# Optimization experiments

Hardware: AMD Instinct MI355X
Metric: run time of the kernel (lower is better)

## Reference

```python
import jax, jax.numpy as jnp
import numpy as np

NEG_INF = -jnp.inf


def _rope(x, cos, sin):
    # x: (B, S, H, D); cos/sin: (1, S, 1, D//2)
    xr = x.reshape(*x.shape[:-1], -1, 2)
    x1, x2 = xr[..., 0], xr[..., 1]  # (B, S, H, D//2) each
    # faithful to source: concat halves along last axis, same total size D
    return jnp.concatenate([x1 * cos - x2 * sin, x1 * sin + x2 * cos], axis=-1)


def setup_inputs() -> dict:
    B, S, D, H, Ld = 2, 2048, 2048, 16, 128
    key = jax.random.key(0)
    ks = jax.random.split(key, 6)
    sc = 1.0 / np.sqrt(D)
    return {
        "x": jax.random.normal(ks[0], (B, S, D), jnp.float32),
        "attn_mask": jnp.ones((B, S), jnp.int32),
        "Wq": jax.random.normal(ks[1], (D, H * Ld), jnp.float32) * sc,
        "bq": jnp.zeros((H * Ld,), jnp.float32),
        "Wk": jax.random.normal(ks[2], (D, H * Ld), jnp.float32) * sc,
        "bk": jnp.zeros((H * Ld,), jnp.float32),
        "Wv": jax.random.normal(ks[3], (D, H * Ld), jnp.float32) * sc,
        "bv": jnp.zeros((H * Ld,), jnp.float32),
        "Wo": jax.random.normal(ks[4], (H * Ld, D), jnp.float32) * sc,
        "bo": jnp.zeros((D,), jnp.float32),
        "num_heads": H,
    }


def reference(x, attn_mask, Wq, bq, Wk, bk, Wv, bv, Wo, bo, num_heads):
    B, S, D = x.shape
    H = int(num_heads)
    Ld = Wq.shape[1] // H
    base = 10000

    q = (x @ Wq + bq).reshape(B, S, H, Ld)
    k = (x @ Wk + bk).reshape(B, S, H, Ld)
    v = (x @ Wv + bv).reshape(B, S, H, Ld)

    # rotary tables (match RotaryEmbedding.setup, sliced to seq_len)
    inv_freq = 1.0 / base ** (2 * jnp.arange(0, Ld // 2) / Ld)
    angles = jnp.arange(S)[:, None] * inv_freq[None, :]  # (S, Ld//2)
    cos = jnp.cos(angles)[None, :, None, :].astype(x.dtype)
    sin = jnp.sin(angles)[None, :, None, :].astype(x.dtype)
    q = _rope(q, cos, sin)
    k = _rope(k, cos, sin)

    q = jnp.transpose(q, (0, 2, 1, 3))  # (B, H, S, Ld)
    k = jnp.transpose(k, (0, 2, 1, 3))
    v = jnp.transpose(v, (0, 2, 1, 3))

    scale = jnp.sqrt(jnp.float32(Ld)).astype(x.dtype)
    scores = jnp.einsum('bnqd,bnkd->bnqk', q, k) / scale  # (B, H, S, S)

    # faithful mask from source: keep where arange[None,:] >= arange[:,None]
    row_idx = jnp.arange(S)[None, :]
    col_idx = jnp.arange(S)[:, None]
    keep = row_idx >= col_idx  # (S, S)
    scores = jnp.where(keep[None, None, :, :], scores, NEG_INF)

    # padding mask applied over the QUERY axis, as in source: (B,1,S,1)
    scores = jnp.where(attn_mask[:, None, :, None] > 0, scores, NEG_INF)

    attn = jax.nn.softmax(scores, axis=-1)
    attended = jnp.einsum('bnqk,bnkd->bnqd', attn, v)
    attended = jnp.transpose(attended, (0, 2, 1, 3)).reshape(B, S, H * Ld)
    return attended @ Wo + bo
```

## Files before the change

kernel.cpp:

```cpp
#include <hip/hip_runtime.h>
#include <math.h>

typedef __bf16 bf16x8 __attribute__((ext_vector_type(8)));
typedef float f32x4 __attribute__((ext_vector_type(4)));

#define MFMA_BF16(a,b,c) __builtin_amdgcn_mfma_f32_16x16x32_bf16((a),(b),(c),0,0,0)

static constexpr int S_LEN = 2048;
static constexpr int DM    = 2048;
static constexpr int NHEAD = 16;
static constexpr int LDH   = 128;
static constexpr int BATCH = 2;

__device__ __forceinline__ unsigned short f2bf(float f) {
    unsigned u = __float_as_uint(f);
    u += 0x7fffu + ((u >> 16) & 1u);
    return (unsigned short)(u >> 16);
}
__device__ __forceinline__ float bf2f(unsigned short h) {
    return __uint_as_float(((unsigned)h) << 16);
}
__device__ __forceinline__ float fexp2(float x) {
#if __has_builtin(__builtin_amdgcn_exp2f)
    return __builtin_amdgcn_exp2f(x);
#else
    return exp2f(x);
#endif
}

__device__ __forceinline__ void ld_lds16(const void* g, void* l) {
    __builtin_amdgcn_global_load_lds(
        (const __attribute__((address_space(1))) unsigned int*)g,
        (__attribute__((address_space(3))) unsigned int*)l, 16, 0, 0);
}

__global__ void convert_f32_bf16(const float* __restrict__ in,
                                 unsigned short* __restrict__ out, int n4) {
    int idx = blockIdx.x * blockDim.x + threadIdx.x;
    if (idx >= n4) return;
    float4 v = reinterpret_cast<const float4*>(in)[idx];
    unsigned lo = (unsigned)f2bf(v.x) | ((unsigned)f2bf(v.y) << 16);
    unsigned hi = (unsigned)f2bf(v.z) | ((unsigned)f2bf(v.w) << 16);
    reinterpret_cast<uint2*>(out)[idx] = make_uint2(lo, hi);
}

__global__ void wconv_t4(const float* __restrict__ W0, const float* __restrict__ W1,
                         const float* __restrict__ W2, const float* __restrict__ W3,
                         unsigned short* __restrict__ O0, unsigned short* __restrict__ O1,
                         unsigned short* __restrict__ O2, unsigned short* __restrict__ O3) {
    __shared__ unsigned short tile[32][33];
    int z = blockIdx.z;
    const float* W = (z == 0) ? W0 : (z == 1) ? W1 : (z == 2) ? W2 : W3;
    unsigned short* Wt = (z == 0) ? O0 : (z == 1) ? O1 : (z == 2) ? O2 : O3;
    int n0 = blockIdx.x * 32;
    int k0 = blockIdx.y * 32;
    int t = threadIdx.x;
    int ir = t >> 3, ic = (t & 7) * 4;
    float4 v = *reinterpret_cast<const float4*>(&W[(size_t)(k0 + ir) * DM + n0 + ic]);
    tile[ir][ic + 0] = f2bf(v.x);
    tile[ir][ic + 1] = f2bf(v.y);
    tile[ir][ic + 2] = f2bf(v.z);
    tile[ir][ic + 3] = f2bf(v.w);
    __syncthreads();
    unsigned lo = (unsigned)tile[ic + 0][ir] | ((unsigned)tile[ic + 1][ir] << 16);
    unsigned hi = (unsigned)tile[ic + 2][ir] | ((unsigned)tile[ic + 3][ir] << 16);
    *reinterpret_cast<uint2*>(&Wt[(size_t)(n0 + ir) * DM + k0 + ic]) = make_uint2(lo, hi);
}

template<int MODE>
__global__ __launch_bounds__(256, 2) void gemm_bf16(
    const unsigned short* __restrict__ A,
    const unsigned short* __restrict__ Bt,
    const float* __restrict__ b0, const float* __restrict__ b1,
    const float* __restrict__ b2,
    void* __restrict__ outp)
{
    const int K = DM;
    __shared__ __attribute__((aligned(16))) unsigned short As[128 * 32];
    __shared__ __attribute__((aligned(16))) unsigned short Bs[128 * 32];
    int t = threadIdx.x;
    int m0 = blockIdx.y * 128, n0 = blockIdx.x * 128;
    int lane = t & 63, i16 = lane & 15, quad = lane >> 4;
    int w = t >> 6;
    int wm = (w >> 1) * 64, wn = (w & 1) * 64;

    f32x4 acc[4][4];
    const f32x4 z4 = {0.f, 0.f, 0.f, 0.f};
    for (int mi = 0; mi < 4; ++mi)
        for (int ni = 0; ni < 4; ++ni) acc[mi][ni] = z4;

    for (int kk = 0; kk < K; kk += 32) {
        __syncthreads();
#pragma unroll
        for (int j = 0; j < 2; ++j) {
            int off = j * 4096 + w * 1024 + lane * 16;
            int row = off >> 6;
            int g = ((off >> 4) & 3) ^ ((row >> 1) & 3);
            ld_lds16(&A [(size_t)(m0 + row) * K + kk + g * 8], (char*)As + off);
            ld_lds16(&Bt[(size_t)(n0 + row) * K + kk + g * 8], (char*)Bs + off);
        }
        __syncthreads();

        bf16x8 aF[4], bF[4];
#pragma unroll
        for (int mi = 0; mi < 4; ++mi) {
            int rA = wm + mi * 16 + i16;
            aF[mi] = *reinterpret_cast<const bf16x8*>(
                (const char*)As + rA * 64 + ((quad ^ ((rA >> 1) & 3)) * 16));
        }
#pragma unroll
        for (int ni = 0; ni < 4; ++ni) {
            int rB = wn + ni * 16 + i16;
            bF[ni] = *reinterpret_cast<const bf16x8*>(
                (const char*)Bs + rB * 64 + ((quad ^ ((rB >> 1) & 3)) * 16));
        }
#pragma unroll
        for (int mi = 0; mi < 4; ++mi)
#pragma unroll
            for (int ni = 0; ni < 4; ++ni)
                acc[mi][ni] = MFMA_BF16(aF[mi], bF[ni], acc[mi][ni]);
    }

    if constexpr (MODE == 0) {
        __shared__ __attribute__((aligned(16))) unsigned short Cs[128 * 128];
        __syncthreads();
        int which = n0 >> 11;
        const float* bp = (which == 0) ? b0 : ((which == 1) ? b1 : b2);
        for (int mi = 0; mi < 4; ++mi) {
            for (int ni = 0; ni < 4; ++ni) {
                int nl = wn + ni * 16 + i16;
                float bv = bp[(n0 & (DM - 1)) + nl];
                for (int r = 0; r < 4; ++r) {
                    int ml = wm + mi * 16 + quad * 4 + r;
                    Cs[ml * 128 + nl] = f2bf(acc[mi][ni][r] + bv);
                }
            }
        }
        __syncthreads();
        int hh = (n0 & (DM - 1)) >> 7;
#pragma unroll
        for (int it = 0; it < 8; ++it) {
            int idx = it * 256 + t;
            int row = idx >> 4, c16 = idx & 15;
            int mm = m0 + row;
            int bb = mm >> 11, ss = mm & (S_LEN - 1);
            size_t oidx = ((((size_t)which * BATCH + bb) * NHEAD + hh) * S_LEN + ss) * LDH + c16 * 8;
            *reinterpret_cast<uint4*>((unsigned short*)outp + oidx) =
                *reinterpret_cast<const uint4*>(Cs + row * 128 + c16 * 8);
        }
    } else {
        for (int mi = 0; mi < 4; ++mi) {
            for (int ni = 0; ni < 4; ++ni) {
                int nn = n0 + wn + ni * 16 + i16;
                float bv = b0[nn];
                for (int r = 0; r < 4; ++r) {
                    int mm = m0 + wm + mi * 16 + quad * 4 + r;
                    ((float*)outp)[(size_t)mm * DM + nn] = acc[mi][ni][r] + bv;
                }
            }
        }
    }
}

__global__ void rope_kernel(unsigned short* __restrict__ q, unsigned short* __restrict__ k) {
    int w = threadIdx.x >> 6, lane = threadIdx.x & 63;
    int rowid = blockIdx.x * 4 + w;
    bool isq = (rowid < BATCH * NHEAD * S_LEN);
    unsigned short* base = isq ? q : k;
    int idx = rowid & (BATCH * NHEAD * S_LEN - 1);
    int s = idx & (S_LEN - 1);
    unsigned short* row = base + (size_t)idx * LDH;
    unsigned pair = reinterpret_cast<unsigned*>(row)[lane];
    float x1 = bf2f((unsigned short)(pair & 0xffff));
    float x2 = bf2f((unsigned short)(pair >> 16));
    float freq = (float)exp(-(double)(2 * lane) / 128.0 * 9.210340371976184);
    float angle = (float)s * freq;
    float c = cosf(angle), sn = sinf(angle);
    float sc = isq ? (0.08838834764831845f * 1.4426950408889634f) : 1.0f;
    row[lane]      = f2bf((x1 * c - x2 * sn) * sc);
    row[64 + lane] = f2bf((x1 * sn + x2 * c) * sc);
}

__global__ void vtrans(const unsigned short* __restrict__ v, unsigned short* __restrict__ vt) {
    __shared__ unsigned short tile[32][33];
    int bh = blockIdx.z;
    int s0 = blockIdx.x * 32, d0 = blockIdx.y * 32;
    const unsigned short* vin = v + (size_t)bh * S_LEN * LDH;
    unsigned short* vout = vt + (size_t)bh * S_LEN * LDH;
    int t = threadIdx.x;
    int ir = t >> 3, ic = (t & 7) * 4;
    uint2 rv = *reinterpret_cast<const uint2*>(&vin[(size_t)(s0 + ir) * LDH + d0 + ic]);
    tile[ir][ic + 0] = (unsigned short)(rv.x & 0xffff);
    tile[ir][ic + 1] = (unsigned short)(rv.x >> 16);
    tile[ir][ic + 2] = (unsigned short)(rv.y & 0xffff);
    tile[ir][ic + 3] = (unsigned short)(rv.y >> 16);
    __syncthreads();
    unsigned lo = (unsigned)tile[ic + 0][ir] | ((unsigned)tile[ic + 1][ir] << 16);
    unsigned hi = (unsigned)tile[ic + 2][ir] | ((unsigned)tile[ic + 3][ir] << 16);
    *reinterpret_cast<uint2*>(&vout[(size_t)(d0 + ir) * S_LEN + s0 + ic]) = make_uint2(lo, hi);
}

__global__ __launch_bounds__(256, 2) void attn_kernel(
    const unsigned short* __restrict__ q,
    const unsigned short* __restrict__ k,
    const unsigned short* __restrict__ vt,
    unsigned short* __restrict__ att)
{
    __shared__ __attribute__((aligned(16))) unsigned short Ks[64 * 128];
    __shared__ __attribute__((aligned(16))) unsigned short Vs[128 * 64];
    __shared__ __attribute__((aligned(16))) unsigned short Ps[4 * 32 * 64];

    int bid = blockIdx.x;
    int second = bid >> 8;
    int p = bid & 255;
    int xb = second ? (15 - (p >> 5)) : (p >> 5);
    int bh = p & 31;
    int b = bh >> 4, h = bh & (NHEAD - 1);
    int q0 = xb * 128;

    int t = threadIdx.x, w = t >> 6, lane = t & 63;
    int i16 = lane & 15, quad = lane >> 4;
    int qbase = q0 + w * 32;

    bf16x8 qf[2][4];
#pragma unroll
    for (int qs = 0; qs < 2; ++qs) {
        const unsigned short* qrow = q + ((size_t)bh * S_LEN + qbase + qs * 16 + i16) * LDH;
#pragma unroll
        for (int c = 0; c < 4; ++c)
            qf[qs][c] = *reinterpret_cast<const bf16x8*>(qrow + c * 32 + quad * 8);
    }

    const f32x4 z4 = {0.f, 0.f, 0.f, 0.f};
    f32x4 o[2][8];
#pragma unroll
    for (int qs = 0; qs < 2; ++qs)
#pragma unroll
        for (int dt = 0; dt < 8; ++dt) o[qs][dt] = z4;
    float l_i[2] = {0.f, 0.f};

    const unsigned short* kbh  = k  + (size_t)bh * S_LEN * LDH;
    const unsigned short* vtbh = vt + (size_t)bh * LDH * S_LEN;
    unsigned short* PsW = Ps + w * (32 * 64);

    for (int kk0 = q0; kk0 < S_LEN; kk0 += 64) {
        __syncthreads();
#pragma unroll
        for (int j = 0; j < 4; ++j) {
            int off = j * 4096 + w * 1024 + lane * 16;
            int key = off >> 8;
            int gk = ((off >> 4) & 15) ^ (key & 15);
            ld_lds16(&kbh[(size_t)(kk0 + key) * LDH + gk * 8], (char*)Ks + off);
            int d = off >> 7;
            int gv = ((off >> 4) & 7) ^ (d & 7);
            ld_lds16(&vtbh[(size_t)d * S_LEN + kk0 + gv * 8], (char*)Vs + off);
        }
        __syncthreads();

        if (kk0 + 64 <= qbase) continue;

        f32x4 s[2][4];
#pragma unroll
        for (int qs = 0; qs < 2; ++qs)
#pragma unroll
            for (int kn = 0; kn < 4; ++kn) s[qs][kn] = z4;
#pragma unroll
        for (int c = 0; c < 4; ++c) {
            bf16x8 kf[4];
#pragma unroll
            for (int kn = 0; kn < 4; ++kn) {
                int key = kn * 16 + i16;
                int gs = (c * 4 + quad) ^ (key & 15);
                kf[kn] = *reinterpret_cast<const bf16x8*>((const char*)Ks + key * 256 + gs * 16);
            }
#pragma unroll
            for (int qs = 0; qs < 2; ++qs)
#pragma unroll
                for (int kn = 0; kn < 4; ++kn)
                    s[qs][kn] = MFMA_BF16(kf[kn], qf[qs][c], s[qs][kn]);
        }

        bool diag = (kk0 < qbase + 32);
#pragma unroll
        for (int qs = 0; qs < 2; ++qs) {
            int q_local = qs * 16 + i16;
            int qg = qbase + q_local;
#pragma unroll
            for (int kn = 0; kn < 4; ++kn) {
                int keyb = kk0 + kn * 16 + quad * 4;
                float pv[4];
                if (diag) {
#pragma unroll
                    for (int r = 0; r < 4; ++r)
                        pv[r] = (keyb + r >= qg) ? fexp2(s[qs][kn][r]) : 0.f;
                } else {
#pragma unroll
                    for (int r = 0; r < 4; ++r) pv[r] = fexp2(s[qs][kn][r]);
                }
                l_i[qs] += (pv[0] + pv[1]) + (pv[2] + pv[3]);
                unsigned lo = (unsigned)f2bf(pv[0]) | ((unsigned)f2bf(pv[1]) << 16);
                unsigned hi = (unsigned)f2bf(pv[2]) | ((unsigned)f2bf(pv[3]) << 16);
                int g = (kn * 2 + (quad >> 1)) ^ (q_local & 7);
                char* addr = (char*)PsW + q_local * 128 + g * 16 + (quad & 1) * 8;
                *reinterpret_cast<uint2*>(addr) = make_uint2(lo, hi);
            }
        }

#pragma unroll
        for (int hh = 0; hh < 2; ++hh) {
            bf16x8 pf[2];
#pragma unroll
            for (int qs = 0; qs < 2; ++qs) {
                int q_local = qs * 16 + i16;
                int g = (hh * 4 + quad) ^ (q_local & 7);
                pf[qs] = *reinterpret_cast<const bf16x8*>((const char*)PsW + q_local * 128 + g * 16);
            }
#pragma unroll
            for (int dt = 0; dt < 8; ++dt) {
                int d = dt * 16 + i16;
                int gv = (hh * 4 + quad) ^ (d & 7);
                bf16x8 vf = *reinterpret_cast<const bf16x8*>((const char*)Vs + d * 128 + gv * 16);
                o[0][dt] = MFMA_BF16(pf[0], vf, o[0][dt]);
                o[1][dt] = MFMA_BF16(pf[1], vf, o[1][dt]);
            }
        }
    }

#pragma unroll
    for (int qs = 0; qs < 2; ++qs) {
        float lr = l_i[qs];
        lr += __shfl_xor(lr, 16);
        lr += __shfl_xor(lr, 32);
        l_i[qs] = lr;
    }
#pragma unroll
    for (int qs = 0; qs < 2; ++qs) {
#pragma unroll
        for (int r = 0; r < 4; ++r) {
            float lv = __shfl(l_i[qs], quad * 4 + r);
            float inv = 1.0f / lv;
            int qrow = qbase + qs * 16 + quad * 4 + r;
            unsigned short* orow = att + ((size_t)b * S_LEN + qrow) * DM + h * LDH;
#pragma unroll
            for (int dt = 0; dt < 8; ++dt)
                orow[dt * 16 + i16] = f2bf(o[qs][dt][r] * inv);
        }
    }
}

extern "C" void kernel_launch(void* const* d_in, const int* in_sizes, int n_in,
                              void* d_out, int out_size, void* d_ws, size_t ws_size,
                              hipStream_t stream) {
    const float* x  = (const float*)d_in[0];
    const float* Wq = (const float*)d_in[2];
    const float* bq = (const float*)d_in[3];
    const float* Wk = (const float*)d_in[4];
    const float* bk = (const float*)d_in[5];
    const float* Wv = (const float*)d_in[6];
    const float* bv = (const float*)d_in[7];
    const float* Wo = (const float*)d_in[8];
    const float* bo = (const float*)d_in[9];

    char* ws = (char*)d_ws;
    unsigned short* xb  = (unsigned short*)(ws);
    unsigned short* Wqt = (unsigned short*)(ws + 16777216);
    unsigned short* Wkt = (unsigned short*)(ws + 25165824);
    unsigned short* Wvt = (unsigned short*)(ws + 33554432);
    unsigned short* Wot = (unsigned short*)(ws + 41943040);
    unsigned short* qb  = (unsigned short*)(ws + 50331648);
    unsigned short* kb  = (unsigned short*)(ws + 67108864);
    unsigned short* vb  = (unsigned short*)(ws + 83886080);
    unsigned short* vtb = (unsigned short*)(ws + 100663296);
    unsigned short* att = (unsigned short*)(ws + 117440512);

    convert_f32_bf16<<<8192, 256, 0, stream>>>(x, xb, (BATCH * S_LEN * DM) / 4);
    wconv_t4<<<dim3(64, 64, 4), 256, 0, stream>>>(Wq, Wk, Wv, Wo, Wqt, Wkt, Wvt, Wot);

    gemm_bf16<0><<<dim3(3 * DM / 128, (BATCH * S_LEN) / 128), 256, 0, stream>>>(
        xb, Wqt, bq, bk, bv, qb);

    rope_kernel<<<(2 * BATCH * NHEAD * S_LEN) / 4, 256, 0, stream>>>(qb, kb);
    vtrans<<<dim3(S_LEN / 32, LDH / 32, BATCH * NHEAD), 256, 0, stream>>>(vb, vtb);

    attn_kernel<<<512, 256, 0, stream>>>(qb, kb, vtb, att);

    gemm_bf16<1><<<dim3(DM / 128, (BATCH * S_LEN) / 128), 256, 0, stream>>>(
        att, Wot, bo, bo, bo, (float*)d_out);
}
```

Before: 412.3 us.

## Fuse RoPE and V transpose into QKV GEMM epilogue, double-buffer attention K/V

The QKV projection epilogue now applies rotary embedding and the query scale using precomputed cos/sin tables, and writes V already transposed. This removes the separate rope and vtrans kernels and their extra global-memory round trips. The attention kernel double-buffers the K/V tiles in LDS so the next chunk's loads overlap current compute, at the cost of doubled LDS use, which may lower occupancy. A small table-generation kernel is added, and the exp2 helper now calls the generic exp2f.

```diff
diff --git a/kernel.cpp b/kernel.cpp
--- a/kernel.cpp
+++ b/kernel.cpp
@@ -11,6 +11,7 @@
 static constexpr int NHEAD = 16;
 static constexpr int LDH   = 128;
 static constexpr int BATCH = 2;
+static constexpr size_t QKV_SEG = (size_t)BATCH * NHEAD * S_LEN * LDH;
 
 __device__ __forceinline__ unsigned short f2bf(float f) {
     unsigned u = __float_as_uint(f);
@@ -20,13 +21,7 @@
 __device__ __forceinline__ float bf2f(unsigned short h) {
     return __uint_as_float(((unsigned)h) << 16);
 }
-__device__ __forceinline__ float fexp2(float x) {
-#if __has_builtin(__builtin_amdgcn_exp2f)
-    return __builtin_amdgcn_exp2f(x);
-#else
-    return exp2f(x);
-#endif
-}
+__device__ __forceinline__ float fexp2(float x) { return exp2f(x); }
 
 __device__ __forceinline__ void ld_lds16(const void* g, void* l) {
     __builtin_amdgcn_global_load_lds(
@@ -42,6 +37,15 @@
     unsigned lo = (unsigned)f2bf(v.x) | ((unsigned)f2bf(v.y) << 16);
     unsigned hi = (unsigned)f2bf(v.z) | ((unsigned)f2bf(v.w) << 16);
     reinterpret_cast<uint2*>(out)[idx] = make_uint2(lo, hi);
+}
+
+__global__ void gen_tab(float* __restrict__ ct, float* __restrict__ st) {
+    int i = threadIdx.x & 63;
+    int s = blockIdx.x * 4 + (threadIdx.x >> 6);
+    float freq = (float)exp(-(double)(2 * i) / 128.0 * 9.210340371976184);
+    float a = (float)s * freq;
+    ct[s * 64 + i] = cosf(a);
+    st[s * 64 + i] = sinf(a);
 }
 
 __global__ void wconv_t4(const float* __restrict__ W0, const float* __restrict__ W1,
@@ -73,11 +77,14 @@
     const unsigned short* __restrict__ Bt,
     const float* __restrict__ b0, const float* __restrict__ b1,
     const float* __restrict__ b2,
+    const float* __restrict__ ctab, const float* __restrict__ stab,
     void* __restrict__ outp)
 {
     const int K = DM;
-    __shared__ __attribute__((aligned(16))) unsigned short As[128 * 32];
-    __shared__ __attribute__((aligned(16))) unsigned short Bs[128 * 32];
+    constexpr int SMEM_SHORTS = (MODE == 0) ? 16384 : 8192;
+    __shared__ __attribute__((aligned(16))) unsigned short smem[SMEM_SHORTS];
+    unsigned short* As = smem;
+    unsigned short* Bs = smem + 4096;
     int t = threadIdx.x;
     int m0 = blockIdx.y * 128, n0 = blockIdx.x * 128;
     int lane = t & 63, i16 = lane & 15, quad = lane >> 4;
@@ -122,31 +129,76 @@
     }
 
     if constexpr (MODE == 0) {
-        __shared__ __attribute__((aligned(16))) unsigned short Cs[128 * 128];
+        unsigned short* Cs = smem;
         __syncthreads();
         int which = n0 >> 11;
+        int hh = (n0 & (DM - 1)) >> 7;
         const float* bp = (which == 0) ? b0 : ((which == 1) ? b1 : b2);
-        for (int mi = 0; mi < 4; ++mi) {
-            for (int ni = 0; ni < 4; ++ni) {
-                int nl = wn + ni * 16 + i16;
-                float bv = bp[(n0 & (DM - 1)) + nl];
-                for (int r = 0; r < 4; ++r) {
-                    int ml = wm + mi * 16 + quad * 4 + r;
-                    Cs[ml * 128 + nl] = f2bf(acc[mi][ni][r] + bv);
+        if (which == 2) {
+            for (int mi = 0; mi < 4; ++mi)
+                for (int ni = 0; ni < 4; ++ni) {
+                    int d = wn + ni * 16 + i16;
+                    float bv = bp[(n0 & (DM - 1)) + d];
+                    for (int r = 0; r < 4; ++r) {
+                        int sl = wm + mi * 16 + quad * 4 + r;
+                        Cs[d * 128 + (((sl >> 3) ^ (d & 15)) * 8) + (sl & 7)] =
+                            f2bf(acc[mi][ni][r] + bv);
+                    }
                 }
-            }
-        }
-        __syncthreads();
-        int hh = (n0 & (DM - 1)) >> 7;
-#pragma unroll
-        for (int it = 0; it < 8; ++it) {
-            int idx = it * 256 + t;
-            int row = idx >> 4, c16 = idx & 15;
-            int mm = m0 + row;
-            int bb = mm >> 11, ss = mm & (S_LEN - 1);
-            size_t oidx = ((((size_t)which * BATCH + bb) * NHEAD + hh) * S_LEN + ss) * LDH + c16 * 8;
-            *reinterpret_cast<uint4*>((unsigned short*)outp + oidx) =
-                *reinterpret_cast<const uint4*>(Cs + row * 128 + c16 * 8);
+            __syncthreads();
+            int s0 = m0 & (S_LEN - 1), bb = m0 >> 11;
+            unsigned short* vout = (unsigned short*)outp + 2 * QKV_SEG;
+#pragma unroll
+            for (int it = 0; it < 8; ++it) {
+                int idx = it * 256 + t;
+                int d = idx >> 4, sg = idx & 15;
+                uint4 v = *reinterpret_cast<const uint4*>(&Cs[d * 128 + ((sg ^ (d & 15)) * 8)]);
+                size_t oidx = (((size_t)(bb * NHEAD + hh)) * LDH + d) * S_LEN + s0 + sg * 8;
+                *reinterpret_cast<uint4*>(vout + oidx) = v;
+            }
+        } else {
+            for (int mi = 0; mi < 4; ++mi)
+                for (int ni = 0; ni < 4; ++ni) {
+                    int nl = wn + ni * 16 + i16;
+                    float bv = bp[(n0 & (DM - 1)) + nl];
+                    for (int r = 0; r < 4; ++r) {
+                        int ml = wm + mi * 16 + quad * 4 + r;
+                        Cs[ml * 128 + nl] = f2bf(acc[mi][ni][r] + bv);
+                    }
+                }
+            __syncthreads();
+            float qscale = (which == 0) ? (0.08838834764831845f * 1.4426950408889634f) : 1.0f;
+            unsigned short* qout = (unsigned short*)outp + (size_t)which * QKV_SEG;
+#pragma unroll
+            for (int it = 0; it < 8; ++it) {
+                int idx = it * 256 + t;
+                int row = idx >> 4, c16 = idx & 15;
+                int mm = m0 + row;
+                int ss = mm & (S_LEN - 1), bb = mm >> 11;
+                int i8 = (c16 & 7) * 8;
+                const unsigned short* crow = Cs + row * 128 + i8 * 2;
+                uint4 w0 = *reinterpret_cast<const uint4*>(crow);
+                uint4 w1 = *reinterpret_cast<const uint4*>(crow + 8);
+                unsigned pw[8] = {w0.x, w0.y, w0.z, w0.w, w1.x, w1.y, w1.z, w1.w};
+                float4 cA = *reinterpret_cast<const float4*>(&ctab[ss * 64 + i8]);
+                float4 cB = *reinterpret_cast<const float4*>(&ctab[ss * 64 + i8 + 4]);
+                float4 sA = *reinterpret_cast<const float4*>(&stab[ss * 64 + i8]);
+                float4 sB = *reinterpret_cast<const float4*>(&stab[ss * 64 + i8 + 4]);
+                float cv[8] = {cA.x, cA.y, cA.z, cA.w, cB.x, cB.y, cB.z, cB.w};
+                float sv[8] = {sA.x, sA.y, sA.z, sA.w, sB.x, sB.y, sB.z, sB.w};
+                bool hi = (c16 >= 8);
+                unsigned short ov[8];
+#pragma unroll
+                for (int j = 0; j < 8; ++j) {
+                    float xe = bf2f((unsigned short)(pw[j] & 0xffff));
+                    float xo = bf2f((unsigned short)(pw[j] >> 16));
+                    float o = hi ? (xe * sv[j] + xo * cv[j]) : (xe * cv[j] - xo * sv[j]);
+                    ov[j] = f2bf(o * qscale);
+                }
+                size_t oidx = (((size_t)(bb * NHEAD + hh)) * S_LEN + ss) * LDH + c16 * 8;
+                *reinterpret_cast<uint4*>(qout + oidx) =
+                    *reinterpret_cast<const uint4*>(ov);
+            }
         }
     } else {
         for (int mi = 0; mi < 4; ++mi) {
@@ -162,53 +214,15 @@
     }
 }
 
-__global__ void rope_kernel(unsigned short* __restrict__ q, unsigned short* __restrict__ k) {
-    int w = threadIdx.x >> 6, lane = threadIdx.x & 63;
-    int rowid = blockIdx.x * 4 + w;
-    bool isq = (rowid < BATCH * NHEAD * S_LEN);
-    unsigned short* base = isq ? q : k;
-    int idx = rowid & (BATCH * NHEAD * S_LEN - 1);
-    int s = idx & (S_LEN - 1);
-    unsigned short* row = base + (size_t)idx * LDH;
-    unsigned pair = reinterpret_cast<unsigned*>(row)[lane];
-    float x1 = bf2f((unsigned short)(pair & 0xffff));
-    float x2 = bf2f((unsigned short)(pair >> 16));
-    float freq = (float)exp(-(double)(2 * lane) / 128.0 * 9.210340371976184);
-    float angle = (float)s * freq;
-    float c = cosf(angle), sn = sinf(angle);
-    float sc = isq ? (0.08838834764831845f * 1.4426950408889634f) : 1.0f;
-    row[lane]      = f2bf((x1 * c - x2 * sn) * sc);
-    row[64 + lane] = f2bf((x1 * sn + x2 * c) * sc);
-}
-
-__global__ void vtrans(const unsigned short* __restrict__ v, unsigned short* __restrict__ vt) {
-    __shared__ unsigned short tile[32][33];
-    int bh = blockIdx.z;
-    int s0 = blockIdx.x * 32, d0 = blockIdx.y * 32;
-    const unsigned short* vin = v + (size_t)bh * S_LEN * LDH;
-    unsigned short* vout = vt + (size_t)bh * S_LEN * LDH;
-    int t = threadIdx.x;
-    int ir = t >> 3, ic = (t & 7) * 4;
-    uint2 rv = *reinterpret_cast<const uint2*>(&vin[(size_t)(s0 + ir) * LDH + d0 + ic]);
-    tile[ir][ic + 0] = (unsigned short)(rv.x & 0xffff);
-    tile[ir][ic + 1] = (unsigned short)(rv.x >> 16);
-    tile[ir][ic + 2] = (unsigned short)(rv.y & 0xffff);
-    tile[ir][ic + 3] = (unsigned short)(rv.y >> 16);
-    __syncthreads();
-    unsigned lo = (unsigned)tile[ic + 0][ir] | ((unsigned)tile[ic + 1][ir] << 16);
-    unsigned hi = (unsigned)tile[ic + 2][ir] | ((unsigned)tile[ic + 3][ir] << 16);
-    *reinterpret_cast<uint2*>(&vout[(size_t)(d0 + ir) * S_LEN + s0 + ic]) = make_uint2(lo, hi);
-}
-
 __global__ __launch_bounds__(256, 2) void attn_kernel(
     const unsigned short* __restrict__ q,
     const unsigned short* __restrict__ k,
     const unsigned short* __restrict__ vt,
     unsigned short* __restrict__ att)
 {
-    __shared__ __attribute__((aligned(16))) unsigned short Ks[64 * 128];
-    __shared__ __attribute__((aligned(16))) unsigned short Vs[128 * 64];
-    __shared__ __attribute__((aligned(16))) unsigned short Ps[4 * 32 * 64];
+    __shared__ __attribute__((aligned(16))) unsigned short Ks[2][64 * 128];
+    __shared__ __attribute__((aligned(16))) unsigned short Vs[2][128 * 64];
+    __shared__ __attribute__((aligned(16))) unsigned short Ps[4][32 * 64];
 
     int bid = blockIdx.x;
     int second = bid >> 8;
@@ -241,23 +255,30 @@
 
     const unsigned short* kbh  = k  + (size_t)bh * S_LEN * LDH;
     const unsigned short* vtbh = vt + (size_t)bh * LDH * S_LEN;
-    unsigned short* PsW = Ps + w * (32 * 64);
-
-    for (int kk0 = q0; kk0 < S_LEN; kk0 += 64) {
-        __syncthreads();
+    unsigned short* PsW = Ps[w];
+
+    auto stage = [&](int buf, int kk0) {
 #pragma unroll
         for (int j = 0; j < 4; ++j) {
             int off = j * 4096 + w * 1024 + lane * 16;
             int key = off >> 8;
             int gk = ((off >> 4) & 15) ^ (key & 15);
-            ld_lds16(&kbh[(size_t)(kk0 + key) * LDH + gk * 8], (char*)Ks + off);
+            ld_lds16(&kbh[(size_t)(kk0 + key) * LDH + gk * 8], (char*)Ks[buf] + off);
             int d = off >> 7;
             int gv = ((off >> 4) & 7) ^ (d & 7);
-            ld_lds16(&vtbh[(size_t)d * S_LEN + kk0 + gv * 8], (char*)Vs + off);
-        }
+            ld_lds16(&vtbh[(size_t)d * S_LEN + kk0 + gv * 8], (char*)Vs[buf] + off);
+        }
+    };
+
+    stage(0, q0);
+    int nch = (S_LEN - q0) >> 6;
+    for (int ci = 0; ci < nch; ++ci) {
         __syncthreads();
-
+        if (ci + 1 < nch) stage((ci + 1) & 1, q0 + (ci + 1) * 64);
+        int kk0 = q0 + ci * 64;
         if (kk0 + 64 <= qbase) continue;
+        const unsigned short* Kb = Ks[ci & 1];
+        const unsigned short* Vb = Vs[ci & 1];
 
         f32x4 s[2][4];
 #pragma unroll
@@ -271,7 +292,7 @@
             for (int kn = 0; kn < 4; ++kn) {
                 int key = kn * 16 + i16;
                 int gs = (c * 4 + quad) ^ (key & 15);
-                kf[kn] = *reinterpret_cast<const bf16x8*>((const char*)Ks + key * 256 + gs * 16);
+                kf[kn] = *reinterpret_cast<const bf16x8*>((const char*)Kb + key * 256 + gs * 16);
             }
 #pragma unroll
             for (int qs = 0; qs < 2; ++qs)
@@ -319,7 +340,7 @@
             for (int dt = 0; dt < 8; ++dt) {
                 int d = dt * 16 + i16;
                 int gv = (hh * 4 + quad) ^ (d & 7);
-                bf16x8 vf = *reinterpret_cast<const bf16x8*>((const char*)Vs + d * 128 + gv * 16);
+                bf16x8 vf = *reinterpret_cast<const bf16x8*>((const char*)Vb + d * 128 + gv * 16);
                 o[0][dt] = MFMA_BF16(pf[0], vf, o[0][dt]);
                 o[1][dt] = MFMA_BF16(pf[1], vf, o[1][dt]);
             }
@@ -367,23 +388,20 @@
     unsigned short* Wkt = (unsigned short*)(ws + 25165824);
     unsigned short* Wvt = (unsigned short*)(ws + 33554432);
     unsigned short* Wot = (unsigned short*)(ws + 41943040);
-    unsigned short* qb  = (unsigned short*)(ws + 50331648);
-    unsigned short* kb  = (unsigned short*)(ws + 67108864);
-    unsigned short* vb  = (unsigned short*)(ws + 83886080);
-    unsigned short* vtb = (unsigned short*)(ws + 100663296);
-    unsigned short* att = (unsigned short*)(ws + 117440512);
+    unsigned short* qkv = (unsigned short*)(ws + 50331648);
+    unsigned short* att = (unsigned short*)(ws + 100663296);
+    float* ctab = (float*)(ws + 117440512);
+    float* stab = (float*)(ws + 117964800);
 
     convert_f32_bf16<<<8192, 256, 0, stream>>>(x, xb, (BATCH * S_LEN * DM) / 4);
+    gen_tab<<<512, 256, 0, stream>>>(ctab, stab);
     wconv_t4<<<dim3(64, 64, 4), 256, 0, stream>>>(Wq, Wk, Wv, Wo, Wqt, Wkt, Wvt, Wot);
 
     gemm_bf16<0><<<dim3(3 * DM / 128, (BATCH * S_LEN) / 128), 256, 0, stream>>>(
-        xb, Wqt, bq, bk, bv, qb);
-
-    rope_kernel<<<(2 * BATCH * NHEAD * S_LEN) / 4, 256, 0, stream>>>(qb, kb);
-    vtrans<<<dim3(S_LEN / 32, LDH / 32, BATCH * NHEAD), 256, 0, stream>>>(vb, vtb);
-
-    attn_kernel<<<512, 256, 0, stream>>>(qb, kb, vtb, att);
+        xb, Wqt, bq, bk, bv, ctab, stab, qkv);
+
+    attn_kernel<<<512, 256, 0, stream>>>(qkv, qkv + QKV_SEG, qkv + 2 * QKV_SEG, att);
 
     gemm_bf16<1><<<dim3(DM / 128, (BATCH * S_LEN) / 128), 256, 0, stream>>>(
-        att, Wot, bo, bo, bo, (float*)d_out);
-}
+        att, Wot, bo, bo, bo, ctab, stab, (float*)d_out);
+}
```

After: 407.5 us. No clear change (-1.2%).
